# Performance work log

Hardware: AMD Instinct MI355X
Metric: run time of the kernel (lower is better)

The kernel has to match this reference:

```python
import jax, jax.numpy as jnp
import numpy as np

HID = 256
OUT_DIM = 3


def _nearest_idx(c, size):
    # PyTorch grid_sample nearest, align_corners=False: idx = round(((c+1)*size-1)/2) = floor((c+1)*size/2)
    return jnp.clip(jnp.floor((c + 1.0) * size * 0.5), 0, size - 1).astype(jnp.int32)


def _mlp(x, params):
    # 4 hidden ReLU layers of 256 + linear out (LIIF imnet)
    for w, b in params[:-1]:
        x = jax.nn.relu(x @ w + b)
    w, b = params[-1]
    return x @ w + b


def setup_inputs() -> dict:
    key = jax.random.key(0)
    ks = jax.random.split(key, 16)
    B, C, H, W = 2, 64, 128, 128
    Q = 65536  # 256x256 HR queries
    feat = jax.random.normal(ks[0], (B, C, H, W), dtype=jnp.float32)
    coord = jax.random.uniform(ks[1], (B, Q, 2), dtype=jnp.float32) * 2.0 - 1.0  # in [-1,1)
    cell = jnp.full((B, Q, 2), 2.0 / 256.0, dtype=jnp.float32)
    in_dim = C * 9 + 2 + 2
    dims = [in_dim, HID, HID, HID, HID, OUT_DIM]
    inp = {"feat": feat, "coord": coord, "cell": cell}
    for i in range(5):
        fan_in = dims[i]
        inp[f"w{i}"] = jax.random.normal(ks[2 + 2 * i], (dims[i], dims[i + 1]), dtype=jnp.float32) / np.sqrt(fan_in)
        inp[f"b{i}"] = jnp.zeros((dims[i + 1],), dtype=jnp.float32)
    return inp


def reference(feat, coord, cell, w0, b0, w1, b1, w2, b2, w3, b3, w4, b4):
    params = [(w0, b0), (w1, b1), (w2, b2), (w3, b3), (w4, b4)]
    B, C, H, W = feat.shape
    dt = feat.dtype
    # feat_unfold: F.unfold(feat, 3, padding=1) -> channel order c*9 + (ki*3+kj)
    p = jnp.pad(feat, ((0, 0), (0, 0), (1, 1), (1, 1)))
    feat_u = jnp.stack([p[:, :, i:i + H, j:j + W] for i in range(3) for j in range(3)], axis=2)
    feat_flat = feat_u.reshape(B, C * 9, H * W)  # [B, 576, H*W]

    rx = 1.0 / H  # 2/H/2
    ry = 1.0 / W
    eps_shift = 1e-6
    lim = 1.0 - 1e-6
    rel_cell = cell * jnp.array([H, W], dtype=dt)

    preds, areas = [], []
    for vx in (-1.0, 1.0):
        for vy in (-1.0, 1.0):
            cx = jnp.clip(coord[..., 0] + vx * rx + eps_shift, -lim, lim)
            cy = jnp.clip(coord[..., 1] + vy * ry + eps_shift, -lim, lim)
            ix = _nearest_idx(cx, H)  # coord dim 0 -> height, grid is coord.flip(-1)
            iy = _nearest_idx(cy, W)
            lin = ix * W + iy  # [B, Q]
            q_feat = jnp.take_along_axis(feat_flat, lin[:, None, :], axis=2).transpose(0, 2, 1)  # [B,Q,576]
            # feat_coord grid-center values at the gathered cell (nearest gather of make_coord)
            qx = -1.0 + (2.0 * ix.astype(dt) + 1.0) / H
            qy = -1.0 + (2.0 * iy.astype(dt) + 1.0) / W
            rel = jnp.stack([(coord[..., 0] - qx) * H, (coord[..., 1] - qy) * W], axis=-1)  # [B,Q,2]
            mlp_in = jnp.concatenate([q_feat, rel, rel_cell], axis=-1)  # [B,Q,580]
            preds.append(_mlp(mlp_in, params))  # [B,Q,3]
            areas.append(jnp.abs(rel[..., 0] * rel[..., 1]) + 1e-9)

    # local_ensemble: swap diagonal areas
    areas[0], areas[3] = areas[3], areas[0]
    areas[1], areas[2] = areas[2], areas[1]
    tot = areas[0] + areas[1] + areas[2] + areas[3]
    ret = sum(pr * (a / tot)[..., None] for pr, a in zip(preds, areas))
    return ret
```

## Files before the change

### kernel.cpp

```cpp
#include <hip/hip_runtime.h>

typedef _Float16 half_t;
typedef _Float16 half4 __attribute__((ext_vector_type(4)));
typedef _Float16 half8 __attribute__((ext_vector_type(8)));
typedef float float4v __attribute__((ext_vector_type(4)));

#define MFMA16(a, b, c) __builtin_amdgcn_mfma_f32_16x16x32_f16(a, b, c, 0, 0, 0)

__global__ void pack_all(const float* __restrict__ w0, const float* __restrict__ w1,
                         const float* __restrict__ w2, const float* __restrict__ w3,
                         const float* __restrict__ w4, half_t* __restrict__ w0p,
                         half_t* __restrict__ w1p, half_t* __restrict__ w2p,
                         half_t* __restrict__ w3p, half_t* __restrict__ w4p,
                         half_t* __restrict__ wtp) {
  const int bb = blockIdx.x;
  const float* w;
  half_t* out;
  int K, Nw, nks, base;
  if (bb < 576) {
    w = w0; out = w0p; K = 576; Nw = 256; nks = 18; base = 0;
  } else if (bb < 832) {
    w = w1; out = w1p; K = 256; Nw = 256; nks = 8; base = 576;
  } else if (bb < 1088) {
    w = w2; out = w2p; K = 256; Nw = 256; nks = 8; base = 832;
  } else if (bb < 1344) {
    w = w3; out = w3p; K = 256; Nw = 256; nks = 8; base = 1088;
  } else if (bb < 1360) {
    w = w4; out = w4p; K = 256; Nw = 3; nks = 8; base = 1344;
  } else {
    const int id = threadIdx.x;
#pragma unroll
    for (int e = 0; e < 4; e++) wtp[e * 256 + id] = (half_t)w0[576 * 256 + e * 256 + id];
    return;
  }
  const int id = (bb - base) * 256 + threadIdx.x;
  const int j = id & 7;
  const int lane = (id >> 3) & 63;
  const int t3 = id >> 9;
  const int ks = t3 % nks;
  const int nt = t3 / nks;
  const int n = nt * 16 + (lane & 15);
  const int k = ks * 32 + ((lane >> 4) << 3) + j;
  float v = (k < K && n < Nw) ? w[k * Nw + n] : 0.0f;
  out[id] = (half_t)v;
}

__global__ __launch_bounds__(256, 2) void conv_l0(
    const float* __restrict__ feat, const half_t* __restrict__ w0p,
    const float* __restrict__ b0, half_t* __restrict__ Z) {
  __shared__ alignas(16) half_t Xc[2][64][40];
  const int tid = threadIdx.x;
  const int lane = tid & 63, wave = tid >> 6, quad = lane >> 4, l15 = lane & 15;
  const int blk = blockIdx.x;
  const int b = blk >> 8;
  const int h = (blk >> 1) & 127;
  const int wbase = (blk & 1) << 6;
  const float* featB = feat + b * (64 * 128 * 128);

  auto stage = [&](int ks, int buf) {
#pragma unroll
    for (int e = 0; e < 2; e++) {
      const int idx = e * 256 + tid;
      const int row = idx & 63;
      const int cp = idx >> 6;
      half4 hv;
#pragma unroll
      for (int u = 0; u < 4; u++) {
        const int kk = ks * 32 + cp * 4 + u;
        const int c = kk / 9;
        const int w9 = kk - c * 9;
        const int di = w9 / 3;
        const int dj = w9 - di * 3;
        const int y = h + di - 1;
        const int x = wbase + row + dj - 1;
        float v = 0.0f;
        if ((unsigned)y < 128u && (unsigned)x < 128u) v = featB[(c << 14) + (y << 7) + x];
        hv[u] = (half_t)v;
      }
      *(half4*)(&Xc[buf][row][cp * 4]) = hv;
    }
  };

  const float4v zero4 = {0.0f, 0.0f, 0.0f, 0.0f};
  float4v acc[4][4];
#pragma unroll
  for (int mt = 0; mt < 4; mt++)
#pragma unroll
    for (int jn = 0; jn < 4; jn++) acc[mt][jn] = zero4;

  half8 bcur[4], bnxt[4];
#pragma unroll
  for (int jn = 0; jn < 4; jn++)
    bcur[jn] = *(const half8*)(w0p + ((((wave * 4 + jn) * 18 + 0) * 64 + lane) << 3));
  stage(0, 0);
  __syncthreads();

#pragma unroll 1
  for (int ks = 0; ks < 18; ks++) {
    const int buf = ks & 1;
    if (ks + 1 < 18) {
      stage(ks + 1, buf ^ 1);
#pragma unroll
      for (int jn = 0; jn < 4; jn++)
        bnxt[jn] =
            *(const half8*)(w0p + ((((wave * 4 + jn) * 18 + ks + 1) * 64 + lane) << 3));
    }
    half8 a[4];
#pragma unroll
    for (int mt = 0; mt < 4; mt++)
      a[mt] = *(const half8*)(&Xc[buf][mt * 16 + l15][quad * 8]);
#pragma unroll
    for (int mt = 0; mt < 4; mt++)
#pragma unroll
      for (int jn = 0; jn < 4; jn++)
        acc[mt][jn] = MFMA16(bcur[jn], a[mt], acc[mt][jn]);
#pragma unroll
    for (int jn = 0; jn < 4; jn++) bcur[jn] = bnxt[jn];
    __syncthreads();
  }

  const int posbase = b * 16384 + h * 128 + wbase;
#pragma unroll
  for (int jn = 0; jn < 4; jn++) {
    const float4v bb4 = *(const float4v*)(b0 + wave * 64 + jn * 16 + quad * 4);
#pragma unroll
    for (int mt = 0; mt < 4; mt++) {
      half4 hv;
#pragma unroll
      for (int rr = 0; rr < 4; rr++) hv[rr] = (half_t)(acc[mt][jn][rr] + bb4[rr]);
      *(half4*)(&Z[(size_t)(posbase + mt * 16 + l15) * 256 + wave * 64 + jn * 16 +
                   quad * 4]) = hv;
    }
  }
}

__global__ __launch_bounds__(256, 2) void liif_main(
    const float* __restrict__ coord, const float* __restrict__ cell,
    const half_t* __restrict__ Zp, const half_t* __restrict__ wtp,
    const half_t* __restrict__ w1p, const half_t* __restrict__ w2p,
    const half_t* __restrict__ w3p, const half_t* __restrict__ w4p,
    const float* __restrict__ b1, const float* __restrict__ b2,
    const float* __restrict__ b3, const float* __restrict__ b4,
    float* __restrict__ outp) {
  __shared__ alignas(16) half_t Hs[128][264];
  __shared__ float S4[4][128][4];
  __shared__ int pos4[4][64];
  __shared__ half_t relxh[4][64], relyh[4][64];
  __shared__ half_t cellxh[64], cellyh[64];
  __shared__ float area4[4][64];
  __shared__ float oacc[64][4];
  __shared__ float totv[64];

  const int tid = threadIdx.x;
  const int lane = tid & 63;
  const int wave = tid >> 6;
  const int quad = lane >> 4;
  const int l15 = lane & 15;
  const int blk = blockIdx.x;
  const int batch = blk >> 10;

  {
    const int t = tid >> 6, row = tid & 63;
    const int gq = blk * 64 + row;
    const float cx0 = coord[gq * 2 + 0], cy0 = coord[gq * 2 + 1];
    const float vx = (t & 2) ? 1.0f : -1.0f;
    const float vy = (t & 1) ? 1.0f : -1.0f;
    const float r = 1.0f / 128.0f, lim = 1.0f - 1e-6f, eps = 1e-6f;
    float cx = fminf(fmaxf(cx0 + vx * r + eps, -lim), lim);
    float cy = fminf(fmaxf(cy0 + vy * r + eps, -lim), lim);
    int ix = (int)floorf((cx + 1.0f) * 64.0f);
    ix = min(max(ix, 0), 127);
    int iy = (int)floorf((cy + 1.0f) * 64.0f);
    iy = min(max(iy, 0), 127);
    float qx = -1.0f + (2.0f * ix + 1.0f) * (1.0f / 128.0f);
    float qy = -1.0f + (2.0f * iy + 1.0f) * (1.0f / 128.0f);
    float rxv = (cx0 - qx) * 128.0f;
    float ryv = (cy0 - qy) * 128.0f;
    pos4[t][row] = (batch << 14) + (ix << 7) + iy;
    relxh[t][row] = (half_t)rxv;
    relyh[t][row] = (half_t)ryv;
    area4[t][row] = fabsf(rxv * ryv) + 1e-9f;
    if (t == 0) {
      cellxh[row] = (half_t)(cell[gq * 2 + 0] * 128.0f);
      cellyh[row] = (half_t)(cell[gq * 2 + 1] * 128.0f);
      oacc[row][0] = 0.0f;
      oacc[row][1] = 0.0f;
      oacc[row][2] = 0.0f;
      totv[row] = 0.0f;
    }
  }
  __syncthreads();

  const float4v zero4 = {0.0f, 0.0f, 0.0f, 0.0f};
  const half8 zero8 = {0, 0, 0, 0, 0, 0, 0, 0};
  const int c8 = tid & 31;
  const int rbase = (tid >> 5) * 16;

  const half8 wt0 = *(const half8*)(wtp + 0 * 256 + c8 * 8);
  const half8 wt1 = *(const half8*)(wtp + 1 * 256 + c8 * 8);
  const half8 wt2 = *(const half8*)(wtp + 2 * 256 + c8 * 8);
  const half8 wt3 = *(const half8*)(wtp + 3 * 256 + c8 * 8);

  half8 bcur[4], bnxt[4], bf4[2];
#pragma unroll
  for (int jn = 0; jn < 4; jn++)
    bcur[jn] = *(const half8*)(w1p + ((((wave * 4 + jn) * 8 + 0) * 64 + lane) << 3));

#pragma unroll 1
  for (int p = 0; p < 2; p++) {
#pragma unroll
    for (int e = 0; e < 16; e++) {
      const int r = rbase + e;
      const int corner = 2 * p + (r >> 6);
      const int qrow = r & 63;
      const half8 z = *(const half8*)(Zp + ((size_t)pos4[corner][qrow] << 8) + c8 * 8);
      const half_t rx = relxh[corner][qrow], ry = relyh[corner][qrow];
      const half_t cx = cellxh[qrow], cy = cellyh[qrow];
      const half8 rx8 = {rx, rx, rx, rx, rx, rx, rx, rx};
      const half8 ry8 = {ry, ry, ry, ry, ry, ry, ry, ry};
      const half8 cx8 = {cx, cx, cx, cx, cx, cx, cx, cx};
      const half8 cy8 = {cy, cy, cy, cy, cy, cy, cy, cy};
      half8 v = z + rx8 * wt0 + ry8 * wt1 + cx8 * wt2 + cy8 * wt3;
      v = __builtin_elementwise_max(v, zero8);
      *(half8*)(&Hs[r][c8 * 8]) = v;
    }
    __syncthreads();

    float4v acc[8][4];
#pragma unroll 1
    for (int L = 0; L < 3; L++) {
      const half_t* wp = (L == 0) ? w1p : (L == 1) ? w2p : w3p;
      const float* bp = (L == 0) ? b1 : (L == 1) ? b2 : b3;
#pragma unroll
      for (int mt = 0; mt < 8; mt++)
#pragma unroll
        for (int jn = 0; jn < 4; jn++) acc[mt][jn] = zero4;
#pragma unroll 1
      for (int ks = 0; ks < 8; ks++) {
        if (ks + 1 < 8) {
#pragma unroll
          for (int jn = 0; jn < 4; jn++)
            bnxt[jn] =
                *(const half8*)(wp + ((((wave * 4 + jn) * 8 + ks + 1) * 64 + lane) << 3));
        }
        half8 a[8];
#pragma unroll
        for (int mt = 0; mt < 8; mt++)
          a[mt] = *(const half8*)(&Hs[mt * 16 + l15][ks * 32 + quad * 8]);
#pragma unroll
        for (int mt = 0; mt < 8; mt++)
#pragma unroll
          for (int jn = 0; jn < 4; jn++)
            acc[mt][jn] = MFMA16(bcur[jn], a[mt], acc[mt][jn]);
#pragma unroll
        for (int jn = 0; jn < 4; jn++) bcur[jn] = bnxt[jn];
      }
      __syncthreads();
      if (L < 2) {
        const half_t* wpn = (L == 0) ? w2p : w3p;
#pragma unroll
        for (int jn = 0; jn < 4; jn++)
          bcur[jn] = *(const half8*)(wpn + ((((wave * 4 + jn) * 8 + 0) * 64 + lane) << 3));
      } else {
#pragma unroll
        for (int kx = 0; kx < 2; kx++)
          bf4[kx] = *(const half8*)(w4p + (((wave * 2 + kx) * 64 + lane) << 3));
      }
#pragma unroll
      for (int jn = 0; jn < 4; jn++) {
        const float4v bb4 = *(const float4v*)(bp + wave * 64 + jn * 16 + quad * 4);
#pragma unroll
        for (int mt = 0; mt < 8; mt++) {
          half4 hv;
#pragma unroll
          for (int rr = 0; rr < 4; rr++)
            hv[rr] = (half_t)fmaxf(acc[mt][jn][rr] + bb4[rr], 0.0f);
          *(half4*)(&Hs[mt * 16 + l15][wave * 64 + jn * 16 + quad * 4]) = hv;
        }
      }
      __syncthreads();
    }

    float4v acc4[8];
#pragma unroll
    for (int mt = 0; mt < 8; mt++) acc4[mt] = zero4;
#pragma unroll
    for (int kx = 0; kx < 2; kx++) {
      const int ks = wave * 2 + kx;
#pragma unroll
      for (int mt = 0; mt < 8; mt++) {
        half8 a = *(const half8*)(&Hs[mt * 16 + l15][ks * 32 + quad * 8]);
        acc4[mt] = MFMA16(a, bf4[kx], acc4[mt]);
      }
    }
    if (l15 < 4) {
#pragma unroll
      for (int mt = 0; mt < 8; mt++)
#pragma unroll
        for (int rr = 0; rr < 4; rr++)
          S4[wave][mt * 16 + quad * 4 + rr][l15] = acc4[mt][rr];
    }
    __syncthreads();

    if (p == 0) {
#pragma unroll
      for (int jn = 0; jn < 4; jn++)
        bcur[jn] = *(const half8*)(w1p + ((((wave * 4 + jn) * 8 + 0) * 64 + lane) << 3));
    }

    if (tid < 192) {
      const int qrow = tid / 3;
      const int j = tid - qrow * 3;
      const int ca = 2 * p, cb = 2 * p + 1;
      float pa = b4[j] + S4[0][qrow][j] + S4[1][qrow][j] + S4[2][qrow][j] + S4[3][qrow][j];
      float pb = b4[j] + S4[0][qrow + 64][j] + S4[1][qrow + 64][j] +
                 S4[2][qrow + 64][j] + S4[3][qrow + 64][j];
      oacc[qrow][j] += pa * area4[3 - ca][qrow] + pb * area4[3 - cb][qrow];
    } else if (tid < 256) {
      const int qrow = tid - 192;
      totv[qrow] += area4[2 * p][qrow] + area4[2 * p + 1][qrow];
    }
    __syncthreads();
  }

  if (tid < 192) {
    const int qrow = tid / 3;
    const int j = tid - qrow * 3;
    const int gq = blk * 64 + qrow;
    outp[gq * 3 + j] = oacc[qrow][j] / totv[qrow];
  }
}

extern "C" void kernel_launch(void* const* d_in, const int* in_sizes, int n_in,
                              void* d_out, int out_size, void* d_ws, size_t ws_size,
                              hipStream_t stream) {
  const float* feat = (const float*)d_in[0];
  const float* coord = (const float*)d_in[1];
  const float* cell = (const float*)d_in[2];
  const float* w0 = (const float*)d_in[3];
  const float* b0 = (const float*)d_in[4];
  const float* w1 = (const float*)d_in[5];
  const float* b1 = (const float*)d_in[6];
  const float* w2 = (const float*)d_in[7];
  const float* b2 = (const float*)d_in[8];
  const float* w3 = (const float*)d_in[9];
  const float* b3 = (const float*)d_in[10];
  const float* w4 = (const float*)d_in[11];
  const float* b4 = (const float*)d_in[12];

  half_t* w0p = (half_t*)d_ws;
  half_t* w1p = w0p + 147456;
  half_t* w2p = w1p + 65536;
  half_t* w3p = w2p + 65536;
  half_t* w4p = w3p + 65536;
  half_t* wtp = w4p + 4096;
  half_t* Z = (half_t*)d_ws + 524288;

  pack_all<<<1361, 256, 0, stream>>>(w0, w1, w2, w3, w4, w0p, w1p, w2p, w3p, w4p, wtp);
  conv_l0<<<512, 256, 0, stream>>>(feat, w0p, b0, Z);
  liif_main<<<2048, 256, 0, stream>>>(coord, cell, Z, wtp, w1p, w2p, w3p, w4p, b1, b2,
                                      b3, b4, (float*)d_out);
}
```

Before: 336.7 us.

## Restructure MLP and conv kernels so each wave owns its rows and streams weights

After: 514.9 us. 52.9% more time.

```diff
diff --git a/kernel.cpp b/kernel.cpp
--- a/kernel.cpp
+++ b/kernel.cpp
@@ -7,42 +7,63 @@
 
 #define MFMA16(a, b, c) __builtin_amdgcn_mfma_f32_16x16x32_f16(a, b, c, 0, 0, 0)
 
-__global__ void pack_all(const float* __restrict__ w0, const float* __restrict__ w1,
-                         const float* __restrict__ w2, const float* __restrict__ w3,
-                         const float* __restrict__ w4, half_t* __restrict__ w0p,
-                         half_t* __restrict__ w1p, half_t* __restrict__ w2p,
-                         half_t* __restrict__ w3p, half_t* __restrict__ w4p,
-                         half_t* __restrict__ wtp) {
+__global__ __launch_bounds__(256) void pack_frags(
+    const float* __restrict__ w0, const float* __restrict__ w1,
+    const float* __restrict__ w2, const float* __restrict__ w3,
+    const float* __restrict__ w4, half_t* __restrict__ w0p,
+    half_t* __restrict__ w1p, half_t* __restrict__ w2p,
+    half_t* __restrict__ w3p, half_t* __restrict__ w4p,
+    half_t* __restrict__ wtp) {
   const int bb = blockIdx.x;
+  const int tid = threadIdx.x;
+  if (bb == 42) {
+#pragma unroll
+    for (int e = 0; e < 16; e++) {
+      const int id = e * 256 + tid;
+      const int j = id & 7;
+      const int lane = (id >> 3) & 63;
+      const int ks = id >> 9;
+      const int n = lane & 15;
+      const int k = ks * 32 + ((lane >> 4) << 3) + j;
+      w4p[id] = (half_t)((n < 3) ? w4[k * 3 + n] : 0.0f);
+    }
+#pragma unroll
+    for (int e = 0; e < 4; e++)
+      wtp[e * 256 + tid] = (half_t)w0[576 * 256 + e * 256 + tid];
+    return;
+  }
+  __shared__ float Wt[32][260];
   const float* w;
   half_t* out;
-  int K, Nw, nks, base;
-  if (bb < 576) {
-    w = w0; out = w0p; K = 576; Nw = 256; nks = 18; base = 0;
-  } else if (bb < 832) {
-    w = w1; out = w1p; K = 256; Nw = 256; nks = 8; base = 576;
-  } else if (bb < 1088) {
-    w = w2; out = w2p; K = 256; Nw = 256; nks = 8; base = 832;
-  } else if (bb < 1344) {
-    w = w3; out = w3p; K = 256; Nw = 256; nks = 8; base = 1088;
-  } else if (bb < 1360) {
-    w = w4; out = w4p; K = 256; Nw = 3; nks = 8; base = 1344;
-  } else {
-    const int id = threadIdx.x;
-#pragma unroll
-    for (int e = 0; e < 4; e++) wtp[e * 256 + id] = (half_t)w0[576 * 256 + e * 256 + id];
-    return;
-  }
-  const int id = (bb - base) * 256 + threadIdx.x;
-  const int j = id & 7;
-  const int lane = (id >> 3) & 63;
-  const int t3 = id >> 9;
-  const int ks = t3 % nks;
-  const int nt = t3 / nks;
-  const int n = nt * 16 + (lane & 15);
-  const int k = ks * 32 + ((lane >> 4) << 3) + j;
-  float v = (k < K && n < Nw) ? w[k * Nw + n] : 0.0f;
-  out[id] = (half_t)v;
+  int nks, ks;
+  bool reorder = false;
+  if (bb < 18) { w = w0; out = w0p; nks = 18; ks = bb; reorder = true; }
+  else if (bb < 26) { w = w1; out = w1p; nks = 8; ks = bb - 18; }
+  else if (bb < 34) { w = w2; out = w2p; nks = 8; ks = bb - 26; }
+  else { w = w3; out = w3p; nks = 8; ks = bb - 34; }
+  {
+    const int n4 = (tid & 63) * 4;
+    const int kr = tid >> 6;
+#pragma unroll
+    for (int e = 0; e < 8; e++) {
+      const int kp = e * 4 + kr;
+      int kg = ks * 32 + kp;
+      if (reorder) { const int w9 = kg >> 6, c = kg & 63; kg = c * 9 + w9; }
+      *(float4v*)&Wt[kp][n4] = *(const float4v*)(w + (size_t)kg * 256 + n4);
+    }
+  }
+  __syncthreads();
+  const int lane = tid & 63;
+  const int l15 = lane & 15;
+  const int kq = (lane >> 4) << 3;
+#pragma unroll
+  for (int e = 0; e < 4; e++) {
+    const int nt = e * 4 + (tid >> 6);
+    half8 hv;
+#pragma unroll
+    for (int j = 0; j < 8; j++) hv[j] = (half_t)Wt[kq + j][nt * 16 + l15];
+    *(half8*)&out[((nt * nks + ks) * 64 + lane) * 8] = hv;
+  }
 }
 
 __global__ __launch_bounds__(256, 2) void conv_l0(
@@ -57,80 +78,62 @@
   const int wbase = (blk & 1) << 6;
   const float* featB = feat + b * (64 * 128 * 128);
 
+  const int xp = lane & 15;
+  const int g = lane >> 4;
+
   auto stage = [&](int ks, int buf) {
+    const int w9 = ks >> 1;
+    const int di = w9 / 3;
+    const int dj = w9 - 3 * di;
+    const int y = h + di - 1;
+    const int x = wbase + wave * 16 + xp + dj - 1;
+    const bool ok = ((unsigned)y < 128u) && ((unsigned)x < 128u);
+    const float* base = featB + (((ks & 1) << 5) << 14) + (y << 7) + x;
 #pragma unroll
     for (int e = 0; e < 2; e++) {
-      const int idx = e * 256 + tid;
-      const int row = idx & 63;
-      const int cp = idx >> 6;
+      const int klocal = e * 16 + g * 4;
       half4 hv;
 #pragma unroll
       for (int u = 0; u < 4; u++) {
-        const int kk = ks * 32 + cp * 4 + u;
-        const int c = kk / 9;
-        const int w9 = kk - c * 9;
-        const int di = w9 / 3;
-        const int dj = w9 - di * 3;
-        const int y = h + di - 1;
-        const int x = wbase + row + dj - 1;
         float v = 0.0f;
-        if ((unsigned)y < 128u && (unsigned)x < 128u) v = featB[(c << 14) + (y << 7) + x];
+        if (ok) v = base[(klocal + u) << 14];
         hv[u] = (half_t)v;
       }
-      *(half4*)(&Xc[buf][row][cp * 4]) = hv;
+      *(half4*)&Xc[buf][wave * 16 + xp][klocal] = hv;
     }
   };
 
   const float4v zero4 = {0.0f, 0.0f, 0.0f, 0.0f};
-  float4v acc[4][4];
-#pragma unroll
-  for (int mt = 0; mt < 4; mt++)
-#pragma unroll
-    for (int jn = 0; jn < 4; jn++) acc[mt][jn] = zero4;
-
-  half8 bcur[4], bnxt[4];
-#pragma unroll
-  for (int jn = 0; jn < 4; jn++)
-    bcur[jn] = *(const half8*)(w0p + ((((wave * 4 + jn) * 18 + 0) * 64 + lane) << 3));
+  float4v acc[16];
+#pragma unroll
+  for (int nt = 0; nt < 16; nt++) acc[nt] = zero4;
+
   stage(0, 0);
-  __syncthreads();
-
 #pragma unroll 1
   for (int ks = 0; ks < 18; ks++) {
     const int buf = ks & 1;
-    if (ks + 1 < 18) {
-      stage(ks + 1, buf ^ 1);
-#pragma unroll
-      for (int jn = 0; jn < 4; jn++)
-        bnxt[jn] =
-            *(const half8*)(w0p + ((((wave * 4 + jn) * 18 + ks + 1) * 64 + lane) << 3));
-    }
-    half8 a[4];
-#pragma unroll
-    for (int mt = 0; mt < 4; mt++)
-      a[mt] = *(const half8*)(&Xc[buf][mt * 16 + l15][quad * 8]);
-#pragma unroll
-    for (int mt = 0; mt < 4; mt++)
-#pragma unroll
-      for (int jn = 0; jn < 4; jn++)
-        acc[mt][jn] = MFMA16(bcur[jn], a[mt], acc[mt][jn]);
-#pragma unroll
-    for (int jn = 0; jn < 4; jn++) bcur[jn] = bnxt[jn];
-    __syncthreads();
-  }
-
-  const int posbase = b * 16384 + h * 128 + wbase;
-#pragma unroll
-  for (int jn = 0; jn < 4; jn++) {
-    const float4v bb4 = *(const float4v*)(b0 + wave * 64 + jn * 16 + quad * 4);
-#pragma unroll
-    for (int mt = 0; mt < 4; mt++) {
-      half4 hv;
-#pragma unroll
-      for (int rr = 0; rr < 4; rr++) hv[rr] = (half_t)(acc[mt][jn][rr] + bb4[rr]);
-      *(half4*)(&Z[(size_t)(posbase + mt * 16 + l15) * 256 + wave * 64 + jn * 16 +
-                   quad * 4]) = hv;
-    }
+    if (ks + 1 < 18) stage(ks + 1, buf ^ 1);
+    const half8 xf = *(const half8*)&Xc[buf][wave * 16 + l15][quad * 8];
+#pragma unroll
+    for (int grp = 0; grp < 2; grp++) {
+      half8 wf[8];
+#pragma unroll
+      for (int i = 0; i < 8; i++)
+        wf[i] = *(const half8*)(w0p + (((grp * 8 + i) * 18 + ks) * 64 + lane) * 8);
+#pragma unroll
+      for (int i = 0; i < 8; i++)
+        acc[grp * 8 + i] = MFMA16(wf[i], xf, acc[grp * 8 + i]);
+    }
+  }
+
+  const int posbase = b * 16384 + h * 128 + wbase + wave * 16 + l15;
+#pragma unroll
+  for (int nt = 0; nt < 16; nt++) {
+    const float4v bb4 = *(const float4v*)(b0 + nt * 16 + quad * 4);
+    half4 hv;
+#pragma unroll
+    for (int rr = 0; rr < 4; rr++) hv[rr] = (half_t)(acc[nt][rr] + bb4[rr]);
+    *(half4*)&Z[(size_t)posbase * 256 + nt * 16 + quad * 4] = hv;
   }
 }
 
@@ -143,13 +146,12 @@
     const float* __restrict__ b3, const float* __restrict__ b4,
     float* __restrict__ outp) {
   __shared__ alignas(16) half_t Hs[128][264];
-  __shared__ float S4[4][128][4];
+  __shared__ float Sp[2][128][4];
   __shared__ int pos4[4][64];
   __shared__ half_t relxh[4][64], relyh[4][64];
   __shared__ half_t cellxh[64], cellyh[64];
   __shared__ float area4[4][64];
   __shared__ float oacc[64][4];
-  __shared__ float totv[64];
 
   const int tid = threadIdx.x;
   const int lane = tid & 63;
@@ -186,34 +188,33 @@
       oacc[row][0] = 0.0f;
       oacc[row][1] = 0.0f;
       oacc[row][2] = 0.0f;
-      totv[row] = 0.0f;
     }
   }
   __syncthreads();
 
   const float4v zero4 = {0.0f, 0.0f, 0.0f, 0.0f};
   const half8 zero8 = {0, 0, 0, 0, 0, 0, 0, 0};
-  const int c8 = tid & 31;
-  const int rbase = (tid >> 5) * 16;
+  const int c8 = lane & 31;
+  const int rh = lane >> 5;
 
   const half8 wt0 = *(const half8*)(wtp + 0 * 256 + c8 * 8);
   const half8 wt1 = *(const half8*)(wtp + 1 * 256 + c8 * 8);
   const half8 wt2 = *(const half8*)(wtp + 2 * 256 + c8 * 8);
   const half8 wt3 = *(const half8*)(wtp + 3 * 256 + c8 * 8);
 
-  half8 bcur[4], bnxt[4], bf4[2];
-#pragma unroll
-  for (int jn = 0; jn < 4; jn++)
-    bcur[jn] = *(const half8*)(w1p + ((((wave * 4 + jn) * 8 + 0) * 64 + lane) << 3));
+  const int corner0 = wave >> 1;
+  const int qbase = (wave & 1) * 32;
+  const int rwave = wave * 32;
 
 #pragma unroll 1
   for (int p = 0; p < 2; p++) {
+    const int corner = 2 * p + corner0;
 #pragma unroll
     for (int e = 0; e < 16; e++) {
-      const int r = rbase + e;
-      const int corner = 2 * p + (r >> 6);
-      const int qrow = r & 63;
-      const half8 z = *(const half8*)(Zp + ((size_t)pos4[corner][qrow] << 8) + c8 * 8);
+      const int i = 2 * e + rh;
+      const int qrow = qbase + i;
+      const int pos = pos4[corner][qrow];
+      const half8 z = *(const half8*)(Zp + ((size_t)pos << 8) + c8 * 8);
       const half_t rx = relxh[corner][qrow], ry = relyh[corner][qrow];
       const half_t cx = cellxh[qrow], cy = cellyh[qrow];
       const half8 rx8 = {rx, rx, rx, rx, rx, rx, rx, rx};
@@ -222,112 +223,85 @@
       const half8 cy8 = {cy, cy, cy, cy, cy, cy, cy, cy};
       half8 v = z + rx8 * wt0 + ry8 * wt1 + cx8 * wt2 + cy8 * wt3;
       v = __builtin_elementwise_max(v, zero8);
-      *(half8*)(&Hs[r][c8 * 8]) = v;
-    }
-    __syncthreads();
-
-    float4v acc[8][4];
+      *(half8*)&Hs[rwave + i][c8 * 8] = v;
+    }
+
 #pragma unroll 1
     for (int L = 0; L < 3; L++) {
       const half_t* wp = (L == 0) ? w1p : (L == 1) ? w2p : w3p;
       const float* bp = (L == 0) ? b1 : (L == 1) ? b2 : b3;
-#pragma unroll
-      for (int mt = 0; mt < 8; mt++)
-#pragma unroll
-        for (int jn = 0; jn < 4; jn++) acc[mt][jn] = zero4;
+      float4v acc[2][16];
+#pragma unroll
+      for (int mt = 0; mt < 2; mt++)
+#pragma unroll
+        for (int nt = 0; nt < 16; nt++) acc[mt][nt] = zero4;
 #pragma unroll 1
       for (int ks = 0; ks < 8; ks++) {
-        if (ks + 1 < 8) {
-#pragma unroll
-          for (int jn = 0; jn < 4; jn++)
-            bnxt[jn] =
-                *(const half8*)(wp + ((((wave * 4 + jn) * 8 + ks + 1) * 64 + lane) << 3));
-        }
-        half8 a[8];
-#pragma unroll
-        for (int mt = 0; mt < 8; mt++)
-          a[mt] = *(const half8*)(&Hs[mt * 16 + l15][ks * 32 + quad * 8]);
-#pragma unroll
-        for (int mt = 0; mt < 8; mt++)
-#pragma unroll
-          for (int jn = 0; jn < 4; jn++)
-            acc[mt][jn] = MFMA16(bcur[jn], a[mt], acc[mt][jn]);
-#pragma unroll
-        for (int jn = 0; jn < 4; jn++) bcur[jn] = bnxt[jn];
-      }
-      __syncthreads();
-      if (L < 2) {
-        const half_t* wpn = (L == 0) ? w2p : w3p;
-#pragma unroll
-        for (int jn = 0; jn < 4; jn++)
-          bcur[jn] = *(const half8*)(wpn + ((((wave * 4 + jn) * 8 + 0) * 64 + lane) << 3));
-      } else {
-#pragma unroll
-        for (int kx = 0; kx < 2; kx++)
-          bf4[kx] = *(const half8*)(w4p + (((wave * 2 + kx) * 64 + lane) << 3));
-      }
-#pragma unroll
-      for (int jn = 0; jn < 4; jn++) {
-        const float4v bb4 = *(const float4v*)(bp + wave * 64 + jn * 16 + quad * 4);
-#pragma unroll
-        for (int mt = 0; mt < 8; mt++) {
-          half4 hv;
-#pragma unroll
-          for (int rr = 0; rr < 4; rr++)
-            hv[rr] = (half_t)fmaxf(acc[mt][jn][rr] + bb4[rr], 0.0f);
-          *(half4*)(&Hs[mt * 16 + l15][wave * 64 + jn * 16 + quad * 4]) = hv;
+        const half8 xf0 = *(const half8*)&Hs[rwave + l15][ks * 32 + quad * 8];
+        const half8 xf1 = *(const half8*)&Hs[rwave + 16 + l15][ks * 32 + quad * 8];
+#pragma unroll
+        for (int grp = 0; grp < 2; grp++) {
+          half8 wf[8];
+#pragma unroll
+          for (int i = 0; i < 8; i++)
+            wf[i] = *(const half8*)(wp + (((grp * 8 + i) * 8 + ks) * 64 + lane) * 8);
+#pragma unroll
+          for (int i = 0; i < 8; i++) {
+            const int nt = grp * 8 + i;
+            acc[0][nt] = MFMA16(wf[i], xf0, acc[0][nt]);
+            acc[1][nt] = MFMA16(wf[i], xf1, acc[1][nt]);
+          }
         }
       }
-      __syncthreads();
-    }
-
-    float4v acc4[8];
-#pragma unroll
-    for (int mt = 0; mt < 8; mt++) acc4[mt] = zero4;
-#pragma unroll
-    for (int kx = 0; kx < 2; kx++) {
-      const int ks = wave * 2 + kx;
-#pragma unroll
-      for (int mt = 0; mt < 8; mt++) {
-        half8 a = *(const half8*)(&Hs[mt * 16 + l15][ks * 32 + quad * 8]);
-        acc4[mt] = MFMA16(a, bf4[kx], acc4[mt]);
+#pragma unroll
+      for (int nt = 0; nt < 16; nt++) {
+        const float4v bb4 = *(const float4v*)(bp + nt * 16 + quad * 4);
+        half4 h0, h1;
+#pragma unroll
+        for (int rr = 0; rr < 4; rr++) {
+          h0[rr] = (half_t)fmaxf(acc[0][nt][rr] + bb4[rr], 0.0f);
+          h1[rr] = (half_t)fmaxf(acc[1][nt][rr] + bb4[rr], 0.0f);
+        }
+        *(half4*)&Hs[rwave + l15][nt * 16 + quad * 4] = h0;
+        *(half4*)&Hs[rwave + 16 + l15][nt * 16 + quad * 4] = h1;
       }
     }
+
+    float4v a4[2];
+    a4[0] = zero4;
+    a4[1] = zero4;
+#pragma unroll
+    for (int ks = 0; ks < 8; ks++) {
+      const half8 bf = *(const half8*)(w4p + (ks * 64 + lane) * 8);
+      const half8 a0 = *(const half8*)&Hs[rwave + l15][ks * 32 + quad * 8];
+      const half8 a1 = *(const half8*)&Hs[rwave + 16 + l15][ks * 32 + quad * 8];
+      a4[0] = MFMA16(a0, bf, a4[0]);
+      a4[1] = MFMA16(a1, bf, a4[1]);
+    }
     if (l15 < 4) {
 #pragma unroll
-      for (int mt = 0; mt < 8; mt++)
+      for (int mt = 0; mt < 2; mt++)
 #pragma unroll
         for (int rr = 0; rr < 4; rr++)
-          S4[wave][mt * 16 + quad * 4 + rr][l15] = acc4[mt][rr];
+          Sp[p][rwave + mt * 16 + quad * 4 + rr][l15] = a4[mt][rr];
     }
     __syncthreads();
-
-    if (p == 0) {
-#pragma unroll
-      for (int jn = 0; jn < 4; jn++)
-        bcur[jn] = *(const half8*)(w1p + ((((wave * 4 + jn) * 8 + 0) * 64 + lane) << 3));
-    }
 
     if (tid < 192) {
       const int qrow = tid / 3;
       const int j = tid - qrow * 3;
-      const int ca = 2 * p, cb = 2 * p + 1;
-      float pa = b4[j] + S4[0][qrow][j] + S4[1][qrow][j] + S4[2][qrow][j] + S4[3][qrow][j];
-      float pb = b4[j] + S4[0][qrow + 64][j] + S4[1][qrow + 64][j] +
-                 S4[2][qrow + 64][j] + S4[3][qrow + 64][j];
-      oacc[qrow][j] += pa * area4[3 - ca][qrow] + pb * area4[3 - cb][qrow];
-    } else if (tid < 256) {
-      const int qrow = tid - 192;
-      totv[qrow] += area4[2 * p][qrow] + area4[2 * p + 1][qrow];
-    }
-    __syncthreads();
+      const float pa = b4[j] + Sp[p][qrow][j];
+      const float pb = b4[j] + Sp[p][64 + qrow][j];
+      oacc[qrow][j] += pa * area4[3 - 2 * p][qrow] + pb * area4[2 - 2 * p][qrow];
+    }
   }
 
   if (tid < 192) {
     const int qrow = tid / 3;
     const int j = tid - qrow * 3;
-    const int gq = blk * 64 + qrow;
-    outp[gq * 3 + j] = oacc[qrow][j] / totv[qrow];
+    const float tot =
+        area4[0][qrow] + area4[1][qrow] + area4[2][qrow] + area4[3][qrow];
+    outp[(blk * 64 + qrow) * 3 + j] = oacc[qrow][j] / tot;
   }
 }
 
@@ -356,7 +330,7 @@
   half_t* wtp = w4p + 4096;
   half_t* Z = (half_t*)d_ws + 524288;
 
-  pack_all<<<1361, 256, 0, stream>>>(w0, w1, w2, w3, w4, w0p, w1p, w2p, w3p, w4p, wtp);
+  pack_frags<<<43, 256, 0, stream>>>(w0, w1, w2, w3, w4, w0p, w1p, w2p, w3p, w4p, wtp);
   conv_l0<<<512, 256, 0, stream>>>(feat, w0p, b0, Z);
   liif_main<<<2048, 256, 0, stream>>>(coord, cell, Z, wtp, w1p, w2p, w3p, w4p, b1, b2,
                                       b3, b4, (float*)d_out);
```
